# Performance work log

Hardware: AMD Instinct MI355X
Metric: run time of the kernel (lower is better)

## Reference

```python
import jax, jax.numpy as jnp
import numpy as np

N_NODES = 50000


def _gcn_conv(x, src, dst, W, b, n):
    # PyG GCNConv: linear transform, add self-loops, symmetric norm, scatter-sum, bias.
    h = x @ W  # [N, out]
    loop = jnp.arange(n, dtype=src.dtype)
    s = jnp.concatenate([src, loop])
    d = jnp.concatenate([dst, loop])
    deg = jax.ops.segment_sum(jnp.ones_like(d, dtype=h.dtype), d, num_segments=n)
    dinv = jax.lax.rsqrt(jnp.maximum(deg, 1.0))  # deg >= 1 thanks to self-loops
    norm = dinv[s] * dinv[d]  # [E+N]
    msg = h[s] * norm[:, None]
    out = jax.ops.segment_sum(msg, d, num_segments=n)
    return out + b


def setup_inputs() -> dict:
    key = jax.random.key(0)
    ks = jax.random.split(key, 8)
    N, E = N_NODES, 800000
    d_in, d_hid, d_out = 128, 64, 128
    x = jax.random.normal(ks[0], (N, d_in), dtype=jnp.float32)
    edge_index = jax.random.randint(ks[1], (2, E), 0, N, dtype=jnp.int64)
    s = 1.0 / np.sqrt(d_in)
    W1 = jax.random.normal(ks[2], (d_in, d_hid), dtype=jnp.float32) * s
    b1 = jnp.zeros((d_hid,), dtype=jnp.float32)
    Wl = jax.random.normal(ks[3], (d_hid, d_out), dtype=jnp.float32) * (1.0 / np.sqrt(d_hid))
    bl = jnp.zeros((d_out,), dtype=jnp.float32)
    W2 = jax.random.normal(ks[4], (d_hid, d_out), dtype=jnp.float32) * (1.0 / np.sqrt(d_hid))
    b2 = jnp.zeros((d_out,), dtype=jnp.float32)
    return {"x": x, "edge_index": edge_index, "W1": W1, "b1": b1,
            "Wl": Wl, "bl": bl, "W2": W2, "b2": b2}


def reference(x, edge_index, W1, b1, Wl, bl, W2, b2):
    n = x.shape[0]
    src, dst = edge_index[0], edge_index[1]
    h = _gcn_conv(x, src, dst, W1, b1, n)          # conv1 -> [N, 64]
    x1 = h @ Wl + bl                               # residual linear branch [N, 128]
    h = jax.nn.relu(h)
    out = _gcn_conv(h, src, dst, W2, b2, n)        # conv2 -> [N, 128]
    return out + x + x1
```

## Files before the change

### kernel.cpp

```cpp
#include <hip/hip_runtime.h>
#include <hip/hip_fp16.h>

#define DIN 128
#define DH 64
#define DOUT 128
#define STRIDE 64
#define NPART 8

__global__ __launch_bounds__(256) void k_fill(const int* __restrict__ src,
                                              const int* __restrict__ dst,
                                              int* __restrict__ cnt,
                                              unsigned short* __restrict__ csr,
                                              int E, int n) {
  const int part = blockIdx.x & (NPART - 1);
  const int pb = blockIdx.x >> 3;
  const int nblk = gridDim.x >> 3;
  const int lo = (int)((long)part * n / NPART);
  const int hi = (int)((long)(part + 1) * n / NPART);
  for (int e = pb * 256 + threadIdx.x; e < E; e += nblk * 256) {
    int d = dst[e];
    if (d >= lo && d < hi) {
      int slot = atomicAdd(&cnt[d], 1);
      if (slot < STRIDE) csr[(long)d * STRIDE + slot] = (unsigned short)src[e];
    }
  }
}

__global__ __launch_bounds__(256) void k_gemm1(const float* __restrict__ x,
                                               const float* __restrict__ W1,
                                               __half* __restrict__ h0,
                                               const int* __restrict__ cnt,
                                               float* __restrict__ dinv, int n) {
  const int t = threadIdx.x;
  for (int i = blockIdx.x * 256 + t; i < n; i += gridDim.x * 256)
    dinv[i] = rsqrtf(1.0f + (float)min(cnt[i], STRIDE));

  __shared__ float Ws[DIN * DH];
  __shared__ float xs[32][DIN + 4];
  for (int i = t; i < DIN * DH; i += 256) Ws[i] = W1[i];
  const int row0 = blockIdx.x * 32;
  for (int i = t; i < 32 * (DIN / 4); i += 256) {
    int r = i >> 5;
    int k4 = (i & 31) * 4;
    float4 v = make_float4(0.f, 0.f, 0.f, 0.f);
    int row = row0 + r;
    if (row < n) v = *(const float4*)&x[(long)row * DIN + k4];
    *(float4*)&xs[r][k4] = v;
  }
  __syncthreads();
  const int tc = t & 15, tr = t >> 4;
  const int col4 = tc * 4, r0 = tr * 2;
  float acc[2][4];
#pragma unroll
  for (int r = 0; r < 2; r++)
#pragma unroll
    for (int c = 0; c < 4; c++) acc[r][c] = 0.f;
  for (int k4 = 0; k4 < DIN; k4 += 4) {
    float4 xv[2];
#pragma unroll
    for (int r = 0; r < 2; r++) xv[r] = *(const float4*)&xs[r0 + r][k4];
#pragma unroll
    for (int kk = 0; kk < 4; kk++) {
      float4 wv = *(const float4*)&Ws[(k4 + kk) * DH + col4];
#pragma unroll
      for (int r = 0; r < 2; r++) {
        float xval = (&xv[r].x)[kk];
        acc[r][0] = fmaf(xval, wv.x, acc[r][0]);
        acc[r][1] = fmaf(xval, wv.y, acc[r][1]);
        acc[r][2] = fmaf(xval, wv.z, acc[r][2]);
        acc[r][3] = fmaf(xval, wv.w, acc[r][3]);
      }
    }
  }
#pragma unroll
  for (int r = 0; r < 2; r++) {
    int row = row0 + r0 + r;
    if (row < n) {
      union { uint2 u; __half2 h[2]; } sv;
      sv.h[0] = __floats2half2_rn(acc[r][0], acc[r][1]);
      sv.h[1] = __floats2half2_rn(acc[r][2], acc[r][3]);
      *(uint2*)&h0[(long)row * DH + col4] = sv.u;
    }
  }
}

__global__ __launch_bounds__(256) void k_gather1(const int* __restrict__ cnt,
                                                 const unsigned short* __restrict__ csr,
                                                 const float* __restrict__ dinv,
                                                 const __half* __restrict__ h0,
                                                 const float* __restrict__ b1,
                                                 float* __restrict__ h1,
                                                 __half* __restrict__ r16, int n) {
  long gid = (long)blockIdx.x * 256 + threadIdx.x;
  int node = (int)(gid >> 3);
  if (node >= n) return;
  int l = (int)(gid & 7);
  const float dd = dinv[node];
  const int deg = min(cnt[node], STRIDE);
  const long base = (long)node * STRIDE;
  float acc[8];
#pragma unroll
  for (int k = 0; k < 8; k++) acc[k] = 0.f;

  auto edge = [&](int s) {
    float w = dinv[s] * dd;
    union { uint4 u; __half2 h[4]; } c;
    c.u = *(const uint4*)&h0[(long)s * DH + l * 8];
#pragma unroll
    for (int k = 0; k < 4; k++) {
      float2 f = __half22float2(c.h[k]);
      acc[2 * k] = fmaf(f.x, w, acc[2 * k]);
      acc[2 * k + 1] = fmaf(f.y, w, acc[2 * k + 1]);
    }
  };

  int j = 0;
  for (; j + 4 <= deg; j += 4) {
    ushort4 cs = *(const ushort4*)&csr[base + j];
    edge(cs.x); edge(cs.y); edge(cs.z); edge(cs.w);
  }
  for (; j < deg; j++) edge(csr[base + j]);

  const float w = dd * dd;
  union { uint4 u; __half2 h[4]; } cs;
  cs.u = *(const uint4*)&h0[(long)node * DH + l * 8];
  float4 ba = *(const float4*)&b1[l * 8];
  float4 bb = *(const float4*)&b1[l * 8 + 4];
  float o[8];
#pragma unroll
  for (int k = 0; k < 4; k++) {
    float2 f = __half22float2(cs.h[k]);
    o[2 * k] = f.x * w + acc[2 * k];
    o[2 * k + 1] = f.y * w + acc[2 * k + 1];
  }
  o[0] += ba.x; o[1] += ba.y; o[2] += ba.z; o[3] += ba.w;
  o[4] += bb.x; o[5] += bb.y; o[6] += bb.z; o[7] += bb.w;
  *(float4*)&h1[(long)node * DH + l * 8] = make_float4(o[0], o[1], o[2], o[3]);
  *(float4*)&h1[(long)node * DH + l * 8 + 4] = make_float4(o[4], o[5], o[6], o[7]);
  union { uint4 u; __half2 h[4]; } rv;
#pragma unroll
  for (int k = 0; k < 4; k++)
    rv.h[k] = __floats2half2_rn(fmaxf(o[2 * k], 0.f), fmaxf(o[2 * k + 1], 0.f));
  *(uint4*)&r16[(long)node * DH + l * 8] = rv.u;
}

__global__ __launch_bounds__(256) void k_gather2C(const int* __restrict__ cnt,
                                                  const unsigned short* __restrict__ csr,
                                                  const float* __restrict__ dinv,
                                                  const __half* __restrict__ r16,
                                                  const float* __restrict__ h1,
                                                  const float* __restrict__ Wl,
                                                  const float* __restrict__ W2,
                                                  const float* __restrict__ bl,
                                                  const float* __restrict__ b2,
                                                  const float* __restrict__ x,
                                                  float* __restrict__ out, int n) {
  __shared__ float hs[32][DH + 4];
  const int t = threadIdx.x;
  const int row0 = blockIdx.x * 32;

  {
    const int r = t >> 3;
    const int l = t & 7;
    int node = row0 + r;
    float acc[8];
#pragma unroll
    for (int k = 0; k < 8; k++) acc[k] = 0.f;
    if (node < n) {
      const float dd = dinv[node];
      const int deg = min(cnt[node], STRIDE);
      const long base = (long)node * STRIDE;
      auto edge = [&](int s) {
        float w = dinv[s] * dd;
        union { uint4 u; __half2 h[4]; } c;
        c.u = *(const uint4*)&r16[(long)s * DH + l * 8];
#pragma unroll
        for (int k = 0; k < 4; k++) {
          float2 f = __half22float2(c.h[k]);
          acc[2 * k] = fmaf(f.x, w, acc[2 * k]);
          acc[2 * k + 1] = fmaf(f.y, w, acc[2 * k + 1]);
        }
      };
      int j = 0;
      for (; j + 4 <= deg; j += 4) {
        ushort4 cs = *(const ushort4*)&csr[base + j];
        edge(cs.x); edge(cs.y); edge(cs.z); edge(cs.w);
      }
      for (; j < deg; j++) edge(csr[base + j]);
      const float w = dd * dd;
      union { uint4 u; __half2 h[4]; } cs;
      cs.u = *(const uint4*)&r16[(long)node * DH + l * 8];
#pragma unroll
      for (int k = 0; k < 4; k++) {
        float2 f = __half22float2(cs.h[k]);
        acc[2 * k] = fmaf(f.x, w, acc[2 * k]);
        acc[2 * k + 1] = fmaf(f.y, w, acc[2 * k + 1]);
      }
    }
    *(float4*)&hs[r][l * 8] = make_float4(acc[0], acc[1], acc[2], acc[3]);
    *(float4*)&hs[r][l * 8 + 4] = make_float4(acc[4], acc[5], acc[6], acc[7]);
  }

  const int tc = t & 31, tr = t >> 5;
  const int col4 = tc * 4, r0 = tr * 4;
  float acc[4][4];
#pragma unroll
  for (int r = 0; r < 4; r++)
#pragma unroll
    for (int c = 0; c < 4; c++) acc[r][c] = 0.f;

  __syncthreads();
  for (int k4 = 0; k4 < DH; k4 += 4) {
    float4 hv[4];
#pragma unroll
    for (int r = 0; r < 4; r++) hv[r] = *(const float4*)&hs[r0 + r][k4];
#pragma unroll
    for (int kk = 0; kk < 4; kk++) {
      float4 wv = *(const float4*)&W2[(k4 + kk) * DOUT + col4];
#pragma unroll
      for (int r = 0; r < 4; r++) {
        float hval = (&hv[r].x)[kk];
        acc[r][0] = fmaf(hval, wv.x, acc[r][0]);
        acc[r][1] = fmaf(hval, wv.y, acc[r][1]);
        acc[r][2] = fmaf(hval, wv.z, acc[r][2]);
        acc[r][3] = fmaf(hval, wv.w, acc[r][3]);
      }
    }
  }
  __syncthreads();

  for (int i = t; i < 32 * (DH / 4); i += 256) {
    int r = i >> 4;
    int k4 = (i & 15) * 4;
    float4 v = make_float4(0.f, 0.f, 0.f, 0.f);
    int row = row0 + r;
    if (row < n) v = *(const float4*)&h1[(long)row * DH + k4];
    *(float4*)&hs[r][k4] = v;
  }
  __syncthreads();
  for (int k4 = 0; k4 < DH; k4 += 4) {
    float4 hv[4];
#pragma unroll
    for (int r = 0; r < 4; r++) hv[r] = *(const float4*)&hs[r0 + r][k4];
#pragma unroll
    for (int kk = 0; kk < 4; kk++) {
      float4 wv = *(const float4*)&Wl[(k4 + kk) * DOUT + col4];
#pragma unroll
      for (int r = 0; r < 4; r++) {
        float hval = (&hv[r].x)[kk];
        acc[r][0] = fmaf(hval, wv.x, acc[r][0]);
        acc[r][1] = fmaf(hval, wv.y, acc[r][1]);
        acc[r][2] = fmaf(hval, wv.z, acc[r][2]);
        acc[r][3] = fmaf(hval, wv.w, acc[r][3]);
      }
    }
  }

  float4 blv = *(const float4*)&bl[col4];
  float4 b2v = *(const float4*)&b2[col4];
#pragma unroll
  for (int r = 0; r < 4; r++) {
    int row = row0 + r0 + r;
    if (row < n) {
      float4 xv = *(const float4*)&x[(long)row * DOUT + col4];
      float4 o;
      o.x = xv.x + acc[r][0] + blv.x + b2v.x;
      o.y = xv.y + acc[r][1] + blv.y + b2v.y;
      o.z = xv.z + acc[r][2] + blv.z + b2v.z;
      o.w = xv.w + acc[r][3] + blv.w + b2v.w;
      *(float4*)&out[(long)row * DOUT + col4] = o;
    }
  }
}

extern "C" void kernel_launch(void* const* d_in, const int* in_sizes, int n_in,
                              void* d_out, int out_size, void* d_ws, size_t ws_size,
                              hipStream_t stream) {
  const float* x = (const float*)d_in[0];
  const int* edge_index = (const int*)d_in[1];
  const float* W1 = (const float*)d_in[2];
  const float* b1 = (const float*)d_in[3];
  const float* Wl = (const float*)d_in[4];
  const float* bl = (const float*)d_in[5];
  const float* W2 = (const float*)d_in[6];
  const float* b2 = (const float*)d_in[7];
  float* out = (float*)d_out;

  const int n = in_sizes[0] / DIN;
  const int E = in_sizes[1] / 2;
  const int* src = edge_index;
  const int* dst = edge_index + E;

  char* p = (char*)d_ws;
  auto alloc = [&](size_t bytes) { char* r = p; p += (bytes + 255) & ~(size_t)255; return r; };
  int* cnt = (int*)alloc((size_t)n * 4);
  unsigned short* csr = (unsigned short*)alloc((size_t)n * STRIDE * 2);
  float* dinv = (float*)alloc((size_t)n * 4);
  __half* h0 = (__half*)alloc((size_t)n * DH * 2);
  __half* r16 = (__half*)alloc((size_t)n * DH * 2);
  float* h1 = (float*)alloc((size_t)n * DH * 4);

  const int B = 256;
  hipMemsetAsync(cnt, 0, (size_t)n * sizeof(int), stream);
  k_fill<<<NPART * 256, B, 0, stream>>>(src, dst, cnt, csr, E, n);
  k_gemm1<<<(n + 31) / 32, B, 0, stream>>>(x, W1, h0, cnt, dinv, n);
  k_gather1<<<(int)(((long)n * 8 + B - 1) / B), B, 0, stream>>>(cnt, csr, dinv, h0, b1, h1, r16, n);
  k_gather2C<<<(n + 31) / 32, B, 0, stream>>>(cnt, csr, dinv, r16, h1, Wl, W2, bl, b2, x, out, n);
}
```

Measured before the change: 207.5 us.

## Fold symmetric degree normalization into stored features, dropping dinv and fp32 h1

```diff
diff --git a/kernel.cpp b/kernel.cpp
--- a/kernel.cpp
+++ b/kernel.cpp
@@ -28,13 +28,9 @@
 
 __global__ __launch_bounds__(256) void k_gemm1(const float* __restrict__ x,
                                                const float* __restrict__ W1,
-                                               __half* __restrict__ h0,
                                                const int* __restrict__ cnt,
-                                               float* __restrict__ dinv, int n) {
+                                               __half* __restrict__ h0p, int n) {
   const int t = threadIdx.x;
-  for (int i = blockIdx.x * 256 + t; i < n; i += gridDim.x * 256)
-    dinv[i] = rsqrtf(1.0f + (float)min(cnt[i], STRIDE));
-
   __shared__ float Ws[DIN * DH];
   __shared__ float xs[32][DIN + 4];
   for (int i = t; i < DIN * DH; i += 256) Ws[i] = W1[i];
@@ -76,41 +72,39 @@
   for (int r = 0; r < 2; r++) {
     int row = row0 + r0 + r;
     if (row < n) {
+      float dd = rsqrtf(1.0f + (float)min(cnt[row], STRIDE));
       union { uint2 u; __half2 h[2]; } sv;
-      sv.h[0] = __floats2half2_rn(acc[r][0], acc[r][1]);
-      sv.h[1] = __floats2half2_rn(acc[r][2], acc[r][3]);
-      *(uint2*)&h0[(long)row * DH + col4] = sv.u;
+      sv.h[0] = __floats2half2_rn(acc[r][0] * dd, acc[r][1] * dd);
+      sv.h[1] = __floats2half2_rn(acc[r][2] * dd, acc[r][3] * dd);
+      *(uint2*)&h0p[(long)row * DH + col4] = sv.u;
     }
   }
 }
 
 __global__ __launch_bounds__(256) void k_gather1(const int* __restrict__ cnt,
                                                  const unsigned short* __restrict__ csr,
-                                                 const float* __restrict__ dinv,
-                                                 const __half* __restrict__ h0,
+                                                 const __half* __restrict__ h0p,
                                                  const float* __restrict__ b1,
-                                                 float* __restrict__ h1,
-                                                 __half* __restrict__ r16, int n) {
+                                                 __half* __restrict__ hd, int n) {
   long gid = (long)blockIdx.x * 256 + threadIdx.x;
   int node = (int)(gid >> 3);
   if (node >= n) return;
   int l = (int)(gid & 7);
-  const float dd = dinv[node];
   const int deg = min(cnt[node], STRIDE);
+  const float dd = rsqrtf(1.0f + (float)deg);
   const long base = (long)node * STRIDE;
   float acc[8];
 #pragma unroll
   for (int k = 0; k < 8; k++) acc[k] = 0.f;
 
   auto edge = [&](int s) {
-    float w = dinv[s] * dd;
     union { uint4 u; __half2 h[4]; } c;
-    c.u = *(const uint4*)&h0[(long)s * DH + l * 8];
+    c.u = *(const uint4*)&h0p[(long)s * DH + l * 8];
 #pragma unroll
     for (int k = 0; k < 4; k++) {
       float2 f = __half22float2(c.h[k]);
-      acc[2 * k] = fmaf(f.x, w, acc[2 * k]);
-      acc[2 * k + 1] = fmaf(f.y, w, acc[2 * k + 1]);
+      acc[2 * k] += f.x;
+      acc[2 * k + 1] += f.y;
     }
   };
 
@@ -120,35 +114,25 @@
     edge(cs.x); edge(cs.y); edge(cs.z); edge(cs.w);
   }
   for (; j < deg; j++) edge(csr[base + j]);
-
-  const float w = dd * dd;
-  union { uint4 u; __half2 h[4]; } cs;
-  cs.u = *(const uint4*)&h0[(long)node * DH + l * 8];
+  edge(node);
+
   float4 ba = *(const float4*)&b1[l * 8];
   float4 bb = *(const float4*)&b1[l * 8 + 4];
   float o[8];
-#pragma unroll
-  for (int k = 0; k < 4; k++) {
-    float2 f = __half22float2(cs.h[k]);
-    o[2 * k] = f.x * w + acc[2 * k];
-    o[2 * k + 1] = f.y * w + acc[2 * k + 1];
-  }
-  o[0] += ba.x; o[1] += ba.y; o[2] += ba.z; o[3] += ba.w;
-  o[4] += bb.x; o[5] += bb.y; o[6] += bb.z; o[7] += bb.w;
-  *(float4*)&h1[(long)node * DH + l * 8] = make_float4(o[0], o[1], o[2], o[3]);
-  *(float4*)&h1[(long)node * DH + l * 8 + 4] = make_float4(o[4], o[5], o[6], o[7]);
+  o[0] = acc[0] * dd + ba.x; o[1] = acc[1] * dd + ba.y;
+  o[2] = acc[2] * dd + ba.z; o[3] = acc[3] * dd + ba.w;
+  o[4] = acc[4] * dd + bb.x; o[5] = acc[5] * dd + bb.y;
+  o[6] = acc[6] * dd + bb.z; o[7] = acc[7] * dd + bb.w;
   union { uint4 u; __half2 h[4]; } rv;
 #pragma unroll
   for (int k = 0; k < 4; k++)
-    rv.h[k] = __floats2half2_rn(fmaxf(o[2 * k], 0.f), fmaxf(o[2 * k + 1], 0.f));
-  *(uint4*)&r16[(long)node * DH + l * 8] = rv.u;
+    rv.h[k] = __floats2half2_rn(o[2 * k] * dd, o[2 * k + 1] * dd);
+  *(uint4*)&hd[(long)node * DH + l * 8] = rv.u;
 }
 
 __global__ __launch_bounds__(256) void k_gather2C(const int* __restrict__ cnt,
                                                   const unsigned short* __restrict__ csr,
-                                                  const float* __restrict__ dinv,
-                                                  const __half* __restrict__ r16,
-                                                  const float* __restrict__ h1,
+                                                  const __half* __restrict__ hd,
                                                   const float* __restrict__ Wl,
                                                   const float* __restrict__ W2,
                                                   const float* __restrict__ bl,
@@ -166,19 +150,19 @@
     float acc[8];
 #pragma unroll
     for (int k = 0; k < 8; k++) acc[k] = 0.f;
+    float dd = 0.f;
     if (node < n) {
-      const float dd = dinv[node];
       const int deg = min(cnt[node], STRIDE);
+      dd = rsqrtf(1.0f + (float)deg);
       const long base = (long)node * STRIDE;
       auto edge = [&](int s) {
-        float w = dinv[s] * dd;
         union { uint4 u; __half2 h[4]; } c;
-        c.u = *(const uint4*)&r16[(long)s * DH + l * 8];
+        c.u = *(const uint4*)&hd[(long)s * DH + l * 8];
 #pragma unroll
         for (int k = 0; k < 4; k++) {
           float2 f = __half22float2(c.h[k]);
-          acc[2 * k] = fmaf(f.x, w, acc[2 * k]);
-          acc[2 * k + 1] = fmaf(f.y, w, acc[2 * k + 1]);
+          acc[2 * k] += fmaxf(f.x, 0.f);
+          acc[2 * k + 1] += fmaxf(f.y, 0.f);
         }
       };
       int j = 0;
@@ -187,18 +171,12 @@
         edge(cs.x); edge(cs.y); edge(cs.z); edge(cs.w);
       }
       for (; j < deg; j++) edge(csr[base + j]);
-      const float w = dd * dd;
-      union { uint4 u; __half2 h[4]; } cs;
-      cs.u = *(const uint4*)&r16[(long)node * DH + l * 8];
-#pragma unroll
-      for (int k = 0; k < 4; k++) {
-        float2 f = __half22float2(cs.h[k]);
-        acc[2 * k] = fmaf(f.x, w, acc[2 * k]);
-        acc[2 * k + 1] = fmaf(f.y, w, acc[2 * k + 1]);
-      }
-    }
-    *(float4*)&hs[r][l * 8] = make_float4(acc[0], acc[1], acc[2], acc[3]);
-    *(float4*)&hs[r][l * 8 + 4] = make_float4(acc[4], acc[5], acc[6], acc[7]);
+      edge(node);
+    }
+    *(float4*)&hs[r][l * 8] =
+        make_float4(acc[0] * dd, acc[1] * dd, acc[2] * dd, acc[3] * dd);
+    *(float4*)&hs[r][l * 8 + 4] =
+        make_float4(acc[4] * dd, acc[5] * dd, acc[6] * dd, acc[7] * dd);
   }
 
   const int tc = t & 31, tr = t >> 5;
@@ -229,13 +207,26 @@
   }
   __syncthreads();
 
-  for (int i = t; i < 32 * (DH / 4); i += 256) {
-    int r = i >> 4;
-    int k4 = (i & 15) * 4;
-    float4 v = make_float4(0.f, 0.f, 0.f, 0.f);
+  {
+    const int r = t >> 3;
+    const int l8 = (t & 7) * 8;
     int row = row0 + r;
-    if (row < n) v = *(const float4*)&h1[(long)row * DH + k4];
-    *(float4*)&hs[r][k4] = v;
+    float v[8];
+#pragma unroll
+    for (int k = 0; k < 8; k++) v[k] = 0.f;
+    if (row < n) {
+      float sc = sqrtf(1.0f + (float)min(cnt[row], STRIDE));
+      union { uint4 u; __half2 h[4]; } c;
+      c.u = *(const uint4*)&hd[(long)row * DH + l8];
+#pragma unroll
+      for (int k = 0; k < 4; k++) {
+        float2 f = __half22float2(c.h[k]);
+        v[2 * k] = f.x * sc;
+        v[2 * k + 1] = f.y * sc;
+      }
+    }
+    *(float4*)&hs[r][l8] = make_float4(v[0], v[1], v[2], v[3]);
+    *(float4*)&hs[r][l8 + 4] = make_float4(v[4], v[5], v[6], v[7]);
   }
   __syncthreads();
   for (int k4 = 0; k4 < DH; k4 += 4) {
@@ -295,15 +286,13 @@
   auto alloc = [&](size_t bytes) { char* r = p; p += (bytes + 255) & ~(size_t)255; return r; };
   int* cnt = (int*)alloc((size_t)n * 4);
   unsigned short* csr = (unsigned short*)alloc((size_t)n * STRIDE * 2);
-  float* dinv = (float*)alloc((size_t)n * 4);
-  __half* h0 = (__half*)alloc((size_t)n * DH * 2);
-  __half* r16 = (__half*)alloc((size_t)n * DH * 2);
-  float* h1 = (float*)alloc((size_t)n * DH * 4);
+  __half* h0p = (__half*)alloc((size_t)n * DH * 2);
+  __half* hd = (__half*)alloc((size_t)n * DH * 2);
 
   const int B = 256;
   hipMemsetAsync(cnt, 0, (size_t)n * sizeof(int), stream);
   k_fill<<<NPART * 256, B, 0, stream>>>(src, dst, cnt, csr, E, n);
-  k_gemm1<<<(n + 31) / 32, B, 0, stream>>>(x, W1, h0, cnt, dinv, n);
-  k_gather1<<<(int)(((long)n * 8 + B - 1) / B), B, 0, stream>>>(cnt, csr, dinv, h0, b1, h1, r16, n);
-  k_gather2C<<<(n + 31) / 32, B, 0, stream>>>(cnt, csr, dinv, r16, h1, Wl, W2, bl, b2, x, out, n);
-}
+  k_gemm1<<<(n + 31) / 32, B, 0, stream>>>(x, W1, cnt, h0p, n);
+  k_gather1<<<(int)(((long)n * 8 + B - 1) / B), B, 0, stream>>>(cnt, csr, h0p, b1, hd, n);
+  k_gather2C<<<(n + 31) / 32, B, 0, stream>>>(cnt, csr, hd, Wl, W2, bl, b2, x, out, n);
+}
```

Result: no change. 205.4 us (-1.0%).
